# Optimization experiments

Measured on AMD Instinct MI355X. Metric: run time of the kernel, lower is better.

Reference implementation:

```python
import jax, jax.numpy as jnp
import numpy as np

EPS = 1e-5

def layernorm(x, g, b):
    mu = jnp.mean(x, axis=-1, keepdims=True)
    var = jnp.mean(jnp.square(x - mu), axis=-1, keepdims=True)
    return (x - mu) * jax.lax.rsqrt(var + EPS) * g + b

def setup_inputs() -> dict:
    key = jax.random.key(0)
    B, C, W = 1, 256, 64           # C = x_h_dim = query_dim
    D = 256                        # inner_dim = heads(1) * dim_head(256)
    ks = jax.random.split(key, 32)
    sc = 0.02
    inp = {
        'x': jax.random.normal(ks[0], (B, C, W, W), jnp.float32),
        'h': jax.random.normal(ks[1], (B, C, W, W), jnp.float32),
        's': jax.random.normal(ks[2], (B, C, W, W), jnp.float32),
        'm': jax.random.normal(ks[3], (B, C, W, W), jnp.float32),
        't': jax.random.normal(ks[4], (B, C), jnp.float32),
        'wt': jax.random.normal(ks[5], (C, D), jnp.float32) * sc,
        'bt': jnp.zeros((D,), jnp.float32),
        'wk_x': jax.random.normal(ks[6], (C, D), jnp.float32) * sc,
        'wv_x': jax.random.normal(ks[7], (C, D), jnp.float32) * sc,
        'g_x': jnp.ones((C,), jnp.float32), 'be_x': jnp.zeros((C,), jnp.float32),
        'wk_h': jax.random.normal(ks[8], (C, D), jnp.float32) * sc,
        'wv_h': jax.random.normal(ks[9], (C, D), jnp.float32) * sc,
        'g_h': jnp.ones((C,), jnp.float32), 'be_h': jnp.zeros((C,), jnp.float32),
        'wk_s': jax.random.normal(ks[10], (C, D), jnp.float32) * sc,
        'wv_s': jax.random.normal(ks[11], (C, D), jnp.float32) * sc,
        'g_s': jnp.ones((C,), jnp.float32), 'be_s': jnp.zeros((C,), jnp.float32),
        'wk_m': jax.random.normal(ks[12], (C, D), jnp.float32) * sc,
        'wv_m': jax.random.normal(ks[13], (C, D), jnp.float32) * sc,
        'g_m': jnp.ones((C,), jnp.float32), 'be_m': jnp.zeros((C,), jnp.float32),
        'w_geglu': jax.random.normal(ks[14], (D, 2 * D), jnp.float32) * sc,
        'b_geglu': jnp.zeros((2 * D,), jnp.float32),
        'w_ff2': jax.random.normal(ks[15], (D, D), jnp.float32) * sc,
        'b_ff2': jnp.zeros((D,), jnp.float32),
        'g_res': jnp.ones((D,), jnp.float32), 'be_res': jnp.zeros((D,), jnp.float32),
        'w_out': jax.random.normal(ks[16], (D, C), jnp.float32) * sc,
        'b_out': jnp.zeros((C,), jnp.float32),
        'imageWidth': W,
    }
    return inp

def reference(x, h, s, m, t, wt, bt, wk_x, wv_x, g_x, be_x, wk_h, wv_h, g_h, be_h,
              wk_s, wv_s, g_s, be_s, wk_m, wv_m, g_m, be_m,
              w_geglu, b_geglu, w_ff2, b_ff2, g_res, be_res, w_out, b_out, imageWidth):
    B, C, W, _ = x.shape
    N = W * W
    D = wt.shape[1]
    scale = 1.0 / jnp.sqrt(jnp.float32(D))  # dim_head**-0.5 (heads=1)

    # query: t_transform(t) broadcast over all spatial positions -> [B, N, D]
    q = t @ wt + bt
    query = jnp.broadcast_to(q[:, None, :], (B, N, D))

    def tokens(a):  # b c h w -> b (h w) c
        return a.reshape(B, C, N).transpose(0, 2, 1)

    mods = []
    for a, g, be, wk, wv in ((x, g_x, be_x, wk_x, wv_x), (h, g_h, be_h, wk_h, wv_h),
                             (s, g_s, be_s, wk_s, wv_s), (m, g_m, be_m, wk_m, wv_m)):
        a = layernorm(tokens(a), g, be)
        mods.append((a @ wk, a @ wv))  # (k, v) each [B, N, D]

    sims = [jnp.einsum('bid,bjd->bij', query, k) * scale for k, _ in mods]
    combined = jnp.concatenate(sims, axis=-1)          # [B, N, 4N]
    attn = jax.nn.softmax(combined, axis=-1)
    parts = jnp.split(attn, 4, axis=-1)

    out = sum(jnp.einsum('bij,bjd->bid', a, v) for a, (_, v) in zip(parts, mods))

    # FeedForward(inner_dim, mult=1, glu=True) on layernormed sum
    r = layernorm(out, g_res, be_res)
    gg = r @ w_geglu + b_geglu
    u, gate = jnp.split(gg, 2, axis=-1)
    ff = (u * jax.nn.gelu(gate, approximate=False)) @ w_ff2 + b_ff2

    y = ff @ w_out + b_out                              # [B, N, C]
    return y.transpose(0, 2, 1).reshape(B, C, W, W)
```

## Files before the change

### kernel.cpp

```cpp
#include <hip/hip_runtime.h>
#include <math.h>

#define N_TOK 4096

#define OFF_GU    0
#define OFF_GUP   1024
#define OFF_BUP   1056
#define OFF_PM    1088
#define OFF_PSE   1344
#define OFF_PSR   1600
#define OFF_OUTV  1856
#define OFF_GG    2112
#define OFF_Y     2624
#define OFF_WS    3072
#define OFF_WC    69632

#define TSTRIDE 65

__global__ __launch_bounds__(256) void k0(
    const float* __restrict__ t, const float* __restrict__ wt,
    const float* __restrict__ bt,
    const float* __restrict__ wk0, const float* __restrict__ wk1,
    const float* __restrict__ wk2, const float* __restrict__ wk3,
    const float* __restrict__ g0, const float* __restrict__ g1,
    const float* __restrict__ g2, const float* __restrict__ g3,
    const float* __restrict__ be0, const float* __restrict__ be1,
    const float* __restrict__ be2, const float* __restrict__ be3,
    const float* __restrict__ w_ff2, const float* __restrict__ w_out,
    const float* __restrict__ b_geglu, const float* __restrict__ b_ff2,
    const float* __restrict__ b_out, float* __restrict__ ws) {
  const int gid = blockIdx.x;
  const int tid = threadIdx.x;
  __shared__ float sh[264];

  if (gid < 256) {
    sh[tid] = w_ff2[gid * 256 + tid];
    __syncthreads();
    float acc = 0.f;
    #pragma unroll 8
    for (int d = 0; d < 256; ++d) acc += sh[d] * w_out[d * 256 + tid];
    ws[OFF_WC + gid * 256 + tid] = acc;
  } else if (gid < 288) {
    const int local = gid - 256;
    const int m = local >> 3;
    const int c0 = (local & 7) * 32;
    const float* wk = (m == 0) ? wk0 : (m == 1) ? wk1 : (m == 2) ? wk2 : wk3;
    const float* g  = (m == 0) ? g0  : (m == 1) ? g1  : (m == 2) ? g2  : g3;
    const float* be = (m == 0) ? be0 : (m == 1) ? be1 : (m == 2) ? be2 : be3;

    float acc = bt[tid];
    #pragma unroll 8
    for (int c = 0; c < 256; ++c) acc += t[c] * wt[c * 256 + tid];
    sh[tid] = acc;
    __syncthreads();

    const int w = tid >> 6, lane = tid & 63;
    const float4 qv = ((const float4*)sh)[lane];
    float lGU = 0.f, lBU = 0.f;
    #pragma unroll
    for (int r = 0; r < 8; ++r) {
      int c = c0 + w * 8 + r;
      float4 w4 = ((const float4*)(wk + c * 256))[lane];
      float sdot = w4.x * qv.x + w4.y * qv.y + w4.z * qv.z + w4.w * qv.w;
      for (int o = 32; o > 0; o >>= 1) sdot += __shfl_down(sdot, o, 64);
      if (lane == 0) {
        float u = sdot;
        float gu = g[c] * u;
        ws[OFF_GU + m * 256 + c] = gu;
        lGU += gu;
        lBU += be[c] * u;
      }
    }
    __syncthreads();
    if (lane == 0) { sh[256 + w] = lGU; sh[260 + w] = lBU; }
    __syncthreads();
    if (tid == 0) {
      ws[OFF_GUP + m * 8 + (local & 7)] = sh[256] + sh[257] + sh[258] + sh[259];
      ws[OFF_BUP + m * 8 + (local & 7)] = sh[260] + sh[261] + sh[262] + sh[263];
    }
  } else {
    ws[OFF_OUTV + tid] = 0.0f;
    ws[OFF_GG + tid] = b_geglu[tid];
    ws[OFF_GG + 256 + tid] = b_geglu[256 + tid];
    ws[OFF_Y + tid] = b_out[tid];
  }
}

__global__ __launch_bounds__(256) void k2(
    const float* __restrict__ A0, const float* __restrict__ A1,
    const float* __restrict__ A2, const float* __restrict__ A3,
    float* __restrict__ ws) {
  const int b = blockIdx.x;
  const int m = b >> 6;
  const int jbase = (b & 63) * 64;
  const int tid = threadIdx.x;
  const float* A = (m == 0) ? A0 : (m == 1) ? A1 : (m == 2) ? A2 : A3;

  __shared__ float tile[256 * TSTRIDE];
  __shared__ float gu_sh[256];
  __shared__ float r1[256], r2[256], r3[256];
  __shared__ float simj[64], rinvj[64], muj[64], alj[64];

  gu_sh[tid] = ws[OFF_GU + m * 256 + tid];

  {
    const int cr = tid >> 4;
    const int jf = tid & 15;
    #pragma unroll 4
    for (int it = 0; it < 16; ++it) {
      int c = it * 16 + cr;
      float4 v = *(const float4*)(A + c * N_TOK + jbase + jf * 4);
      int base = c * TSTRIDE + jf * 4;
      tile[base] = v.x; tile[base + 1] = v.y;
      tile[base + 2] = v.z; tile[base + 3] = v.w;
    }
  }
  __syncthreads();

  {
    const int j = tid & 63, q = tid >> 6;
    float s1 = 0.f, s2 = 0.f, s3 = 0.f;
    #pragma unroll 8
    for (int i = 0; i < 64; ++i) {
      int c = q * 64 + i;
      float v = tile[c * TSTRIDE + j];
      s1 += v; s2 += v * v; s3 += v * gu_sh[c];
    }
    r1[tid] = s1; r2[tid] = s2; r3[tid] = s3;
  }
  __syncthreads();
  if (tid < 64) {
    float S1 = r1[tid] + r1[tid + 64] + r1[tid + 128] + r1[tid + 192];
    float S2 = r2[tid] + r2[tid + 64] + r2[tid + 128] + r2[tid + 192];
    float S3 = r3[tid] + r3[tid + 64] + r3[tid + 128] + r3[tid + 192];
    float GU = 0.f, BU = 0.f;
    #pragma unroll
    for (int i = 0; i < 8; ++i) {
      GU += ws[OFF_GUP + m * 8 + i];
      BU += ws[OFF_BUP + m * 8 + i];
    }
    float mu = S1 * (1.0f / 256.0f);
    float var = S2 * (1.0f / 256.0f) - mu * mu;
    float rinv = rsqrtf(var + 1e-5f);
    simj[tid] = 0.0625f * (rinv * (S3 - mu * GU) + BU);
    muj[tid] = mu;
    rinvj[tid] = rinv;
  }
  __syncthreads();
  if (tid < 64) {
    float sim = simj[tid];
    float mb = sim;
    #pragma unroll
    for (int o = 1; o < 64; o <<= 1) mb = fmaxf(mb, __shfl_xor(mb, o, 64));
    float e = expf(sim - mb);
    float al = e * rinvj[tid];
    alj[tid] = al;
    float se = e, sr = al * muj[tid];
    #pragma unroll
    for (int o = 1; o < 64; o <<= 1) {
      se += __shfl_xor(se, o, 64);
      sr += __shfl_xor(sr, o, 64);
    }
    if (tid == 0) {
      ws[OFF_PM + b] = mb;
      ws[OFF_PSE + b] = se;
      ws[OFF_PSR + b] = sr;
    }
  }
  __syncthreads();
  {
    float wsum = 0.f;
    #pragma unroll 8
    for (int j = 0; j < 64; ++j) wsum += alj[j] * tile[tid * TSTRIDE + j];
    ws[OFF_WS + b * 256 + tid] = wsum;
  }
}

__global__ __launch_bounds__(256) void k3(
    const float* __restrict__ wv0, const float* __restrict__ wv1,
    const float* __restrict__ wv2, const float* __restrict__ wv3,
    const float* __restrict__ g0, const float* __restrict__ g1,
    const float* __restrict__ g2, const float* __restrict__ g3,
    const float* __restrict__ be0, const float* __restrict__ be1,
    const float* __restrict__ be2, const float* __restrict__ be3,
    float* __restrict__ ws) {
  const int b = blockIdx.x;
  const int mb = b >> 2;
  const int cbase = (b & 3) * 64;
  const int tid = threadIdx.x;
  const float* wv = (mb == 0) ? wv0 : (mb == 1) ? wv1 : (mb == 2) ? wv2 : wv3;
  const float* g  = (mb == 0) ? g0  : (mb == 1) ? g1  : (mb == 2) ? g2  : g3;
  const float* be = (mb == 0) ? be0 : (mb == 1) ? be1 : (mb == 2) ? be2 : be3;

  __shared__ float pm[256], pse[256], psr[256];
  __shared__ float red[4];
  __shared__ float wfin[64], fsh[64];
  __shared__ float sS, sAm, sPm;

  pm[tid] = ws[OFF_PM + tid];
  pse[tid] = ws[OFF_PSE + tid];
  psr[tid] = ws[OFF_PSR + tid];
  __syncthreads();

  float v = pm[tid];
  for (int o = 32; o > 0; o >>= 1) v = fmaxf(v, __shfl_down(v, o, 64));
  if ((tid & 63) == 0) red[tid >> 6] = v;
  __syncthreads();
  const float M = fmaxf(fmaxf(red[0], red[1]), fmaxf(red[2], red[3]));
  __syncthreads();

  const float f = expf(pm[tid] - M);
  const float fse = f * pse[tid];
  const bool mine = (tid >> 6) == mb;

  v = fse;
  for (int o = 32; o > 0; o >>= 1) v += __shfl_down(v, o, 64);
  if ((tid & 63) == 0) red[tid >> 6] = v;
  __syncthreads();
  if (tid == 0) sS = red[0] + red[1] + red[2] + red[3];
  __syncthreads();
  v = mine ? fse : 0.f;
  for (int o = 32; o > 0; o >>= 1) v += __shfl_down(v, o, 64);
  if ((tid & 63) == 0) red[tid >> 6] = v;
  __syncthreads();
  if (tid == 0) sAm = red[0] + red[1] + red[2] + red[3];
  __syncthreads();
  v = mine ? f * psr[tid] : 0.f;
  for (int o = 32; o > 0; o >>= 1) v += __shfl_down(v, o, 64);
  if ((tid & 63) == 0) red[tid >> 6] = v;
  __syncthreads();
  if (tid == 0) sPm = red[0] + red[1] + red[2] + red[3];
  if (tid < 64) fsh[tid] = expf(pm[mb * 64 + tid] - M);
  __syncthreads();

  const float invS = 1.0f / sS;

  {
    const int c_l = tid & 63, bg = tid >> 6;
    float part = 0.f;
    #pragma unroll 4
    for (int i = 0; i < 16; ++i) {
      int fb = bg * 16 + i;
      part += fsh[fb] * ws[OFF_WS + (mb * 64 + fb) * 256 + cbase + c_l];
    }
    pse[tid] = part;
  }
  __syncthreads();
  if (tid < 64) {
    float dot = (pse[tid] + pse[tid + 64] + pse[tid + 128] + pse[tid + 192]) * invS;
    int c = cbase + tid;
    wfin[tid] = g[c] * (dot - sPm * invS) + be[c] * (sAm * invS);
  }
  __syncthreads();

  {
    float acc = 0.f;
    #pragma unroll 8
    for (int i = 0; i < 64; ++i) acc += wfin[i] * wv[(cbase + i) * 256 + tid];
    atomicAdd(&ws[OFF_OUTV + tid], acc);
  }
}

__global__ __launch_bounds__(256) void k4(
    const float* __restrict__ g_res, const float* __restrict__ be_res,
    const float* __restrict__ w_geglu, float* __restrict__ ws) {
  const int gid = blockIdx.x;
  const int tid = threadIdx.x;
  __shared__ float r_sh[256];
  __shared__ float red[4];

  float od = ws[OFF_OUTV + tid];
  float v = od;
  for (int o = 32; o > 0; o >>= 1) v += __shfl_down(v, o, 64);
  if ((tid & 63) == 0) red[tid >> 6] = v;
  __syncthreads();
  float mu = (red[0] + red[1] + red[2] + red[3]) * (1.0f / 256.0f);
  __syncthreads();
  float dv = od - mu;
  v = dv * dv;
  for (int o = 32; o > 0; o >>= 1) v += __shfl_down(v, o, 64);
  if ((tid & 63) == 0) red[tid >> 6] = v;
  __syncthreads();
  float var = (red[0] + red[1] + red[2] + red[3]) * (1.0f / 256.0f);
  r_sh[tid] = dv * rsqrtf(var + 1e-5f) * g_res[tid] + be_res[tid];
  __syncthreads();

  const int dt = gid >> 4;
  const int d0 = (gid & 15) * 16;
  float acc = 0.f;
  #pragma unroll
  for (int i = 0; i < 16; ++i) {
    int d = d0 + i;
    acc += r_sh[d] * w_geglu[d * 512 + dt * 256 + tid];
  }
  atomicAdd(&ws[OFF_GG + dt * 256 + tid], acc);
}

__global__ __launch_bounds__(256) void k5(
    const float* __restrict__ b_ff2, const float* __restrict__ w_out,
    float* __restrict__ ws) {
  const int gid = blockIdx.x;
  const int tid = threadIdx.x;
  float acc = 0.f;
  if (gid < 16) {
    const int e0 = gid * 16;
    #pragma unroll
    for (int i = 0; i < 16; ++i) {
      int e = e0 + i;
      float u = ws[OFF_GG + e];
      float gate = ws[OFF_GG + 256 + e];
      float ffin = u * 0.5f * gate * (1.0f + erff(gate * 0.70710678118654752f));
      acc += ffin * ws[OFF_WC + e * 256 + tid];
    }
  } else {
    const int d0 = (gid - 16) * 16;
    #pragma unroll
    for (int i = 0; i < 16; ++i) {
      int d = d0 + i;
      acc += b_ff2[d] * w_out[d * 256 + tid];
    }
  }
  atomicAdd(&ws[OFF_Y + tid], acc);
}

__global__ __launch_bounds__(256) void k6(const float* __restrict__ ws,
                                          float4* __restrict__ out4) {
  const int gid = blockIdx.x;
  const int tid = threadIdx.x;
  #pragma unroll
  for (int k = 0; k < 2; ++k) {
    const int idx = gid * 512 + k * 256 + tid;
    const int c = idx >> 10;
    float v = ws[OFF_Y + c];
    out4[idx] = make_float4(v, v, v, v);
  }
}

extern "C" void kernel_launch(void* const* d_in, const int* in_sizes, int n_in,
                              void* d_out, int out_size, void* d_ws, size_t ws_size,
                              hipStream_t stream) {
  const float* x = (const float*)d_in[0];
  const float* h = (const float*)d_in[1];
  const float* s = (const float*)d_in[2];
  const float* m = (const float*)d_in[3];
  const float* t = (const float*)d_in[4];
  const float* wt = (const float*)d_in[5];
  const float* bt = (const float*)d_in[6];
  const float* wk_x = (const float*)d_in[7];
  const float* wv_x = (const float*)d_in[8];
  const float* g_x = (const float*)d_in[9];
  const float* be_x = (const float*)d_in[10];
  const float* wk_h = (const float*)d_in[11];
  const float* wv_h = (const float*)d_in[12];
  const float* g_h = (const float*)d_in[13];
  const float* be_h = (const float*)d_in[14];
  const float* wk_s = (const float*)d_in[15];
  const float* wv_s = (const float*)d_in[16];
  const float* g_s = (const float*)d_in[17];
  const float* be_s = (const float*)d_in[18];
  const float* wk_m = (const float*)d_in[19];
  const float* wv_m = (const float*)d_in[20];
  const float* g_m = (const float*)d_in[21];
  const float* be_m = (const float*)d_in[22];
  const float* w_geglu = (const float*)d_in[23];
  const float* b_geglu = (const float*)d_in[24];
  const float* w_ff2 = (const float*)d_in[25];
  const float* b_ff2 = (const float*)d_in[26];
  const float* g_res = (const float*)d_in[27];
  const float* be_res = (const float*)d_in[28];
  const float* w_out = (const float*)d_in[29];
  const float* b_out = (const float*)d_in[30];
  float* ws = (float*)d_ws;

  k0<<<dim3(289), dim3(256), 0, stream>>>(t, wt, bt,
      wk_x, wk_h, wk_s, wk_m, g_x, g_h, g_s, g_m, be_x, be_h, be_s, be_m,
      w_ff2, w_out, b_geglu, b_ff2, b_out, ws);
  k2<<<dim3(256), dim3(256), 0, stream>>>(x, h, s, m, ws);
  k3<<<dim3(16), dim3(256), 0, stream>>>(wv_x, wv_h, wv_s, wv_m,
      g_x, g_h, g_s, g_m, be_x, be_h, be_s, be_m, ws);
  k4<<<dim3(32), dim3(256), 0, stream>>>(g_res, be_res, w_geglu, ws);
  k5<<<dim3(32), dim3(256), 0, stream>>>(b_ff2, w_out, ws);
  k6<<<dim3(512), dim3(256), 0, stream>>>(ws, (float4*)d_out);
}
```

Before: 163.3 us.

## Fuse all stages into one cooperative kernel with grid syncs

Merges the six separate launches into a single cooperative kernel of 256 blocks. The stages are separated by grid-wide barriers, and the 256 blocks and shared-memory buffers are reused across stages. Atomic accumulations into the workspace are replaced by per-block partial buffers that the next stage sums. The folded b_ff2·w_out bias is now computed up front. The aim is to remove per-launch overhead and atomic contention. In exchange it adds five grid.sync barriers and makes every stage run with the larger shared-memory footprint, which may limit occupancy.

```diff
diff --git a/kernel.cpp b/kernel.cpp
--- a/kernel.cpp
+++ b/kernel.cpp
@@ -1,7 +1,11 @@
 #include <hip/hip_runtime.h>
+#include <hip/hip_cooperative_groups.h>
 #include <math.h>
 
+namespace cg = cooperative_groups;
+
 #define N_TOK 4096
+#define TSTRIDE 65
 
 #define OFF_GU    0
 #define OFF_GUP   1024
@@ -9,53 +13,62 @@
 #define OFF_PM    1088
 #define OFF_PSE   1344
 #define OFF_PSR   1600
-#define OFF_OUTV  1856
-#define OFF_GG    2112
-#define OFF_Y     2624
-#define OFF_WS    3072
-#define OFF_WC    69632
-
-#define TSTRIDE 65
-
-__global__ __launch_bounds__(256) void k0(
+#define OFF_YB    1856
+#define OFF_OUTP  2112
+#define OFF_GGP   6208
+#define OFF_YP    14400
+#define OFF_WS    18496
+#define OFF_WC    84032
+
+__global__ __launch_bounds__(256) void fused(
+    const float* __restrict__ xg, const float* __restrict__ hg,
+    const float* __restrict__ sg, const float* __restrict__ mg,
     const float* __restrict__ t, const float* __restrict__ wt,
     const float* __restrict__ bt,
     const float* __restrict__ wk0, const float* __restrict__ wk1,
     const float* __restrict__ wk2, const float* __restrict__ wk3,
+    const float* __restrict__ wv0, const float* __restrict__ wv1,
+    const float* __restrict__ wv2, const float* __restrict__ wv3,
     const float* __restrict__ g0, const float* __restrict__ g1,
     const float* __restrict__ g2, const float* __restrict__ g3,
     const float* __restrict__ be0, const float* __restrict__ be1,
     const float* __restrict__ be2, const float* __restrict__ be3,
-    const float* __restrict__ w_ff2, const float* __restrict__ w_out,
-    const float* __restrict__ b_geglu, const float* __restrict__ b_ff2,
-    const float* __restrict__ b_out, float* __restrict__ ws) {
-  const int gid = blockIdx.x;
+    const float* __restrict__ w_geglu, const float* __restrict__ b_geglu,
+    const float* __restrict__ w_ff2, const float* __restrict__ b_ff2,
+    const float* __restrict__ g_res, const float* __restrict__ be_res,
+    const float* __restrict__ w_out, const float* __restrict__ b_out,
+    float* __restrict__ ws, float4* __restrict__ out4) {
+  cg::grid_group grid = cg::this_grid();
+  const int b = blockIdx.x;
   const int tid = threadIdx.x;
-  __shared__ float sh[264];
-
-  if (gid < 256) {
-    sh[tid] = w_ff2[gid * 256 + tid];
-    __syncthreads();
+
+  __shared__ float tile[256 * TSTRIDE];
+  __shared__ float sA[256], sB[256], sC[256], sD[256], sE[256];
+  __shared__ float sRed[16];
+
+  sA[tid] = w_ff2[b * 256 + tid];
+  __syncthreads();
+  {
     float acc = 0.f;
     #pragma unroll 8
-    for (int d = 0; d < 256; ++d) acc += sh[d] * w_out[d * 256 + tid];
-    ws[OFF_WC + gid * 256 + tid] = acc;
-  } else if (gid < 288) {
-    const int local = gid - 256;
-    const int m = local >> 3;
-    const int c0 = (local & 7) * 32;
-    const float* wk = (m == 0) ? wk0 : (m == 1) ? wk1 : (m == 2) ? wk2 : wk3;
-    const float* g  = (m == 0) ? g0  : (m == 1) ? g1  : (m == 2) ? g2  : g3;
-    const float* be = (m == 0) ? be0 : (m == 1) ? be1 : (m == 2) ? be2 : be3;
+    for (int d = 0; d < 256; ++d) acc += sA[d] * w_out[d * 256 + tid];
+    ws[OFF_WC + b * 256 + tid] = acc;
+  }
+  if (b < 32) {
+    const int mo = b >> 3;
+    const int c0 = (b & 7) * 32;
+    const float* wk = (mo == 0) ? wk0 : (mo == 1) ? wk1 : (mo == 2) ? wk2 : wk3;
+    const float* g  = (mo == 0) ? g0  : (mo == 1) ? g1  : (mo == 2) ? g2  : g3;
+    const float* be = (mo == 0) ? be0 : (mo == 1) ? be1 : (mo == 2) ? be2 : be3;
 
     float acc = bt[tid];
     #pragma unroll 8
     for (int c = 0; c < 256; ++c) acc += t[c] * wt[c * 256 + tid];
-    sh[tid] = acc;
+    sB[tid] = acc;
     __syncthreads();
 
     const int w = tid >> 6, lane = tid & 63;
-    const float4 qv = ((const float4*)sh)[lane];
+    const float4 qv = ((const float4*)sB)[lane];
     float lGU = 0.f, lBU = 0.f;
     #pragma unroll
     for (int r = 0; r < 8; ++r) {
@@ -66,273 +79,250 @@
       if (lane == 0) {
         float u = sdot;
         float gu = g[c] * u;
-        ws[OFF_GU + m * 256 + c] = gu;
+        ws[OFF_GU + mo * 256 + c] = gu;
         lGU += gu;
         lBU += be[c] * u;
       }
     }
     __syncthreads();
-    if (lane == 0) { sh[256 + w] = lGU; sh[260 + w] = lBU; }
+    if (lane == 0) { sRed[w] = lGU; sRed[8 + w] = lBU; }
     __syncthreads();
     if (tid == 0) {
-      ws[OFF_GUP + m * 8 + (local & 7)] = sh[256] + sh[257] + sh[258] + sh[259];
-      ws[OFF_BUP + m * 8 + (local & 7)] = sh[260] + sh[261] + sh[262] + sh[263];
-    }
-  } else {
-    ws[OFF_OUTV + tid] = 0.0f;
-    ws[OFF_GG + tid] = b_geglu[tid];
-    ws[OFF_GG + 256 + tid] = b_geglu[256 + tid];
-    ws[OFF_Y + tid] = b_out[tid];
-  }
-}
-
-__global__ __launch_bounds__(256) void k2(
-    const float* __restrict__ A0, const float* __restrict__ A1,
-    const float* __restrict__ A2, const float* __restrict__ A3,
-    float* __restrict__ ws) {
-  const int b = blockIdx.x;
-  const int m = b >> 6;
-  const int jbase = (b & 63) * 64;
-  const int tid = threadIdx.x;
-  const float* A = (m == 0) ? A0 : (m == 1) ? A1 : (m == 2) ? A2 : A3;
-
-  __shared__ float tile[256 * TSTRIDE];
-  __shared__ float gu_sh[256];
-  __shared__ float r1[256], r2[256], r3[256];
-  __shared__ float simj[64], rinvj[64], muj[64], alj[64];
-
-  gu_sh[tid] = ws[OFF_GU + m * 256 + tid];
+      ws[OFF_GUP + mo * 8 + (b & 7)] = sRed[0] + sRed[1] + sRed[2] + sRed[3];
+      ws[OFF_BUP + mo * 8 + (b & 7)] = sRed[8] + sRed[9] + sRed[10] + sRed[11];
+    }
+  } else if (b == 32) {
+    float acc = b_out[tid];
+    #pragma unroll 8
+    for (int d = 0; d < 256; ++d) acc += b_ff2[d] * w_out[d * 256 + tid];
+    ws[OFF_YB + tid] = acc;
+  }
+
+  __threadfence();
+  grid.sync();
 
   {
-    const int cr = tid >> 4;
-    const int jf = tid & 15;
-    #pragma unroll 4
-    for (int it = 0; it < 16; ++it) {
-      int c = it * 16 + cr;
-      float4 v = *(const float4*)(A + c * N_TOK + jbase + jf * 4);
-      int base = c * TSTRIDE + jf * 4;
-      tile[base] = v.x; tile[base + 1] = v.y;
-      tile[base + 2] = v.z; tile[base + 3] = v.w;
-    }
-  }
-  __syncthreads();
-
-  {
-    const int j = tid & 63, q = tid >> 6;
-    float s1 = 0.f, s2 = 0.f, s3 = 0.f;
-    #pragma unroll 8
-    for (int i = 0; i < 64; ++i) {
-      int c = q * 64 + i;
-      float v = tile[c * TSTRIDE + j];
-      s1 += v; s2 += v * v; s3 += v * gu_sh[c];
-    }
-    r1[tid] = s1; r2[tid] = s2; r3[tid] = s3;
-  }
-  __syncthreads();
-  if (tid < 64) {
-    float S1 = r1[tid] + r1[tid + 64] + r1[tid + 128] + r1[tid + 192];
-    float S2 = r2[tid] + r2[tid + 64] + r2[tid + 128] + r2[tid + 192];
-    float S3 = r3[tid] + r3[tid + 64] + r3[tid + 128] + r3[tid + 192];
-    float GU = 0.f, BU = 0.f;
-    #pragma unroll
-    for (int i = 0; i < 8; ++i) {
-      GU += ws[OFF_GUP + m * 8 + i];
-      BU += ws[OFF_BUP + m * 8 + i];
-    }
-    float mu = S1 * (1.0f / 256.0f);
-    float var = S2 * (1.0f / 256.0f) - mu * mu;
-    float rinv = rsqrtf(var + 1e-5f);
-    simj[tid] = 0.0625f * (rinv * (S3 - mu * GU) + BU);
-    muj[tid] = mu;
-    rinvj[tid] = rinv;
-  }
-  __syncthreads();
-  if (tid < 64) {
-    float sim = simj[tid];
-    float mb = sim;
-    #pragma unroll
-    for (int o = 1; o < 64; o <<= 1) mb = fmaxf(mb, __shfl_xor(mb, o, 64));
-    float e = expf(sim - mb);
-    float al = e * rinvj[tid];
-    alj[tid] = al;
-    float se = e, sr = al * muj[tid];
-    #pragma unroll
-    for (int o = 1; o < 64; o <<= 1) {
-      se += __shfl_xor(se, o, 64);
-      sr += __shfl_xor(sr, o, 64);
-    }
-    if (tid == 0) {
-      ws[OFF_PM + b] = mb;
-      ws[OFF_PSE + b] = se;
-      ws[OFF_PSR + b] = sr;
-    }
-  }
-  __syncthreads();
-  {
-    float wsum = 0.f;
-    #pragma unroll 8
-    for (int j = 0; j < 64; ++j) wsum += alj[j] * tile[tid * TSTRIDE + j];
-    ws[OFF_WS + b * 256 + tid] = wsum;
-  }
-}
-
-__global__ __launch_bounds__(256) void k3(
-    const float* __restrict__ wv0, const float* __restrict__ wv1,
-    const float* __restrict__ wv2, const float* __restrict__ wv3,
-    const float* __restrict__ g0, const float* __restrict__ g1,
-    const float* __restrict__ g2, const float* __restrict__ g3,
-    const float* __restrict__ be0, const float* __restrict__ be1,
-    const float* __restrict__ be2, const float* __restrict__ be3,
-    float* __restrict__ ws) {
-  const int b = blockIdx.x;
-  const int mb = b >> 2;
-  const int cbase = (b & 3) * 64;
-  const int tid = threadIdx.x;
-  const float* wv = (mb == 0) ? wv0 : (mb == 1) ? wv1 : (mb == 2) ? wv2 : wv3;
-  const float* g  = (mb == 0) ? g0  : (mb == 1) ? g1  : (mb == 2) ? g2  : g3;
-  const float* be = (mb == 0) ? be0 : (mb == 1) ? be1 : (mb == 2) ? be2 : be3;
-
-  __shared__ float pm[256], pse[256], psr[256];
-  __shared__ float red[4];
-  __shared__ float wfin[64], fsh[64];
-  __shared__ float sS, sAm, sPm;
-
-  pm[tid] = ws[OFF_PM + tid];
-  pse[tid] = ws[OFF_PSE + tid];
-  psr[tid] = ws[OFF_PSR + tid];
-  __syncthreads();
-
-  float v = pm[tid];
-  for (int o = 32; o > 0; o >>= 1) v = fmaxf(v, __shfl_down(v, o, 64));
-  if ((tid & 63) == 0) red[tid >> 6] = v;
-  __syncthreads();
-  const float M = fmaxf(fmaxf(red[0], red[1]), fmaxf(red[2], red[3]));
-  __syncthreads();
-
-  const float f = expf(pm[tid] - M);
-  const float fse = f * pse[tid];
-  const bool mine = (tid >> 6) == mb;
-
-  v = fse;
-  for (int o = 32; o > 0; o >>= 1) v += __shfl_down(v, o, 64);
-  if ((tid & 63) == 0) red[tid >> 6] = v;
-  __syncthreads();
-  if (tid == 0) sS = red[0] + red[1] + red[2] + red[3];
-  __syncthreads();
-  v = mine ? fse : 0.f;
-  for (int o = 32; o > 0; o >>= 1) v += __shfl_down(v, o, 64);
-  if ((tid & 63) == 0) red[tid >> 6] = v;
-  __syncthreads();
-  if (tid == 0) sAm = red[0] + red[1] + red[2] + red[3];
-  __syncthreads();
-  v = mine ? f * psr[tid] : 0.f;
-  for (int o = 32; o > 0; o >>= 1) v += __shfl_down(v, o, 64);
-  if ((tid & 63) == 0) red[tid >> 6] = v;
-  __syncthreads();
-  if (tid == 0) sPm = red[0] + red[1] + red[2] + red[3];
-  if (tid < 64) fsh[tid] = expf(pm[mb * 64 + tid] - M);
-  __syncthreads();
-
-  const float invS = 1.0f / sS;
-
-  {
-    const int c_l = tid & 63, bg = tid >> 6;
-    float part = 0.f;
-    #pragma unroll 4
-    for (int i = 0; i < 16; ++i) {
-      int fb = bg * 16 + i;
-      part += fsh[fb] * ws[OFF_WS + (mb * 64 + fb) * 256 + cbase + c_l];
-    }
-    pse[tid] = part;
-  }
-  __syncthreads();
-  if (tid < 64) {
-    float dot = (pse[tid] + pse[tid + 64] + pse[tid + 128] + pse[tid + 192]) * invS;
-    int c = cbase + tid;
-    wfin[tid] = g[c] * (dot - sPm * invS) + be[c] * (sAm * invS);
-  }
-  __syncthreads();
-
-  {
+    const int mo = b >> 6;
+    const int jbase = (b & 63) * 64;
+    const float* A = (mo == 0) ? xg : (mo == 1) ? hg : (mo == 2) ? sg : mg;
+
+    sA[tid] = ws[OFF_GU + mo * 256 + tid];
+    {
+      const int cr = tid >> 4;
+      const int jf = tid & 15;
+      #pragma unroll 4
+      for (int it = 0; it < 16; ++it) {
+        int c = it * 16 + cr;
+        float4 v4 = *(const float4*)(A + c * N_TOK + jbase + jf * 4);
+        int base = c * TSTRIDE + jf * 4;
+        tile[base] = v4.x; tile[base + 1] = v4.y;
+        tile[base + 2] = v4.z; tile[base + 3] = v4.w;
+      }
+    }
+    __syncthreads();
+
+    {
+      const int j = tid & 63, q = tid >> 6;
+      float s1 = 0.f, s2 = 0.f, s3 = 0.f;
+      #pragma unroll 8
+      for (int i = 0; i < 64; ++i) {
+        int c = q * 64 + i;
+        float v = tile[c * TSTRIDE + j];
+        s1 += v; s2 += v * v; s3 += v * sA[c];
+      }
+      sB[tid] = s1; sC[tid] = s2; sD[tid] = s3;
+    }
+    __syncthreads();
+    if (tid < 64) {
+      float S1 = sB[tid] + sB[tid + 64] + sB[tid + 128] + sB[tid + 192];
+      float S2 = sC[tid] + sC[tid + 64] + sC[tid + 128] + sC[tid + 192];
+      float S3 = sD[tid] + sD[tid + 64] + sD[tid + 128] + sD[tid + 192];
+      float GU = 0.f, BU = 0.f;
+      #pragma unroll
+      for (int i = 0; i < 8; ++i) {
+        GU += ws[OFF_GUP + mo * 8 + i];
+        BU += ws[OFF_BUP + mo * 8 + i];
+      }
+      float mu = S1 * (1.0f / 256.0f);
+      float var = S2 * (1.0f / 256.0f) - mu * mu;
+      float rinv = rsqrtf(var + 1e-5f);
+      sE[tid] = 0.0625f * (rinv * (S3 - mu * GU) + BU);
+      sE[64 + tid] = rinv;
+      sE[128 + tid] = mu;
+    }
+    __syncthreads();
+    if (tid < 64) {
+      float sim = sE[tid];
+      float mb_ = sim;
+      #pragma unroll
+      for (int o = 1; o < 64; o <<= 1) mb_ = fmaxf(mb_, __shfl_xor(mb_, o, 64));
+      float e = expf(sim - mb_);
+      float al = e * sE[64 + tid];
+      sE[192 + tid] = al;
+      float se = e, sr = al * sE[128 + tid];
+      #pragma unroll
+      for (int o = 1; o < 64; o <<= 1) {
+        se += __shfl_xor(se, o, 64);
+        sr += __shfl_xor(sr, o, 64);
+      }
+      if (tid == 0) {
+        ws[OFF_PM + b] = mb_;
+        ws[OFF_PSE + b] = se;
+        ws[OFF_PSR + b] = sr;
+      }
+    }
+    __syncthreads();
+    {
+      float wsum = 0.f;
+      #pragma unroll 8
+      for (int j = 0; j < 64; ++j) wsum += sE[192 + j] * tile[tid * TSTRIDE + j];
+      ws[OFF_WS + b * 256 + tid] = wsum;
+    }
+  }
+
+  __threadfence();
+  grid.sync();
+
+  if (b < 16) {
+    const int mb = b >> 2;
+    const int cbase = (b & 3) * 64;
+    const float* wv = (mb == 0) ? wv0 : (mb == 1) ? wv1 : (mb == 2) ? wv2 : wv3;
+    const float* g  = (mb == 0) ? g0  : (mb == 1) ? g1  : (mb == 2) ? g2  : g3;
+    const float* be = (mb == 0) ? be0 : (mb == 1) ? be1 : (mb == 2) ? be2 : be3;
+
+    sA[tid] = ws[OFF_PM + tid];
+    sB[tid] = ws[OFF_PSE + tid];
+    sC[tid] = ws[OFF_PSR + tid];
+    __syncthreads();
+
+    float v = sA[tid];
+    for (int o = 32; o > 0; o >>= 1) v = fmaxf(v, __shfl_down(v, o, 64));
+    if ((tid & 63) == 0) sRed[tid >> 6] = v;
+    __syncthreads();
+    const float M = fmaxf(fmaxf(sRed[0], sRed[1]), fmaxf(sRed[2], sRed[3]));
+    __syncthreads();
+
+    const float f = expf(sA[tid] - M);
+    const float fse = f * sB[tid];
+    const bool mine = (tid >> 6) == mb;
+
+    v = fse;
+    for (int o = 32; o > 0; o >>= 1) v += __shfl_down(v, o, 64);
+    if ((tid & 63) == 0) sRed[tid >> 6] = v;
+    __syncthreads();
+    if (tid == 0) sRed[8] = sRed[0] + sRed[1] + sRed[2] + sRed[3];
+    __syncthreads();
+    v = mine ? fse : 0.f;
+    for (int o = 32; o > 0; o >>= 1) v += __shfl_down(v, o, 64);
+    if ((tid & 63) == 0) sRed[tid >> 6] = v;
+    __syncthreads();
+    if (tid == 0) sRed[9] = sRed[0] + sRed[1] + sRed[2] + sRed[3];
+    __syncthreads();
+    v = mine ? f * sC[tid] : 0.f;
+    for (int o = 32; o > 0; o >>= 1) v += __shfl_down(v, o, 64);
+    if ((tid & 63) == 0) sRed[tid >> 6] = v;
+    __syncthreads();
+    if (tid == 0) sRed[10] = sRed[0] + sRed[1] + sRed[2] + sRed[3];
+    if (tid < 64) sD[64 + tid] = expf(sA[mb * 64 + tid] - M);
+    __syncthreads();
+
+    const float invS = 1.0f / sRed[8];
+
+    {
+      const int c_l = tid & 63, bg = tid >> 6;
+      float part = 0.f;
+      #pragma unroll 4
+      for (int i = 0; i < 16; ++i) {
+        int fb = bg * 16 + i;
+        part += sD[64 + fb] * ws[OFF_WS + (mb * 64 + fb) * 256 + cbase + c_l];
+      }
+      sB[tid] = part;
+    }
+    __syncthreads();
+    if (tid < 64) {
+      float dot = (sB[tid] + sB[tid + 64] + sB[tid + 128] + sB[tid + 192]) * invS;
+      int c = cbase + tid;
+      sD[tid] = g[c] * (dot - sRed[10] * invS) + be[c] * (sRed[9] * invS);
+    }
+    __syncthreads();
+
+    {
+      float acc = 0.f;
+      #pragma unroll 8
+      for (int i = 0; i < 64; ++i) acc += sD[i] * wv[(cbase + i) * 256 + tid];
+      ws[OFF_OUTP + b * 256 + tid] = acc;
+    }
+  }
+
+  __threadfence();
+  grid.sync();
+
+  if (b < 32) {
+    float od = 0.f;
+    #pragma unroll
+    for (int i = 0; i < 16; ++i) od += ws[OFF_OUTP + i * 256 + tid];
+
+    float v = od;
+    for (int o = 32; o > 0; o >>= 1) v += __shfl_down(v, o, 64);
+    if ((tid & 63) == 0) sRed[tid >> 6] = v;
+    __syncthreads();
+    float mu = (sRed[0] + sRed[1] + sRed[2] + sRed[3]) * (1.0f / 256.0f);
+    __syncthreads();
+    float dv = od - mu;
+    v = dv * dv;
+    for (int o = 32; o > 0; o >>= 1) v += __shfl_down(v, o, 64);
+    if ((tid & 63) == 0) sRed[tid >> 6] = v;
+    __syncthreads();
+    float var = (sRed[0] + sRed[1] + sRed[2] + sRed[3]) * (1.0f / 256.0f);
+    sA[tid] = dv * rsqrtf(var + 1e-5f) * g_res[tid] + be_res[tid];
+    __syncthreads();
+
+    const int dt = b >> 4;
+    const int d0 = (b & 15) * 16;
     float acc = 0.f;
-    #pragma unroll 8
-    for (int i = 0; i < 64; ++i) acc += wfin[i] * wv[(cbase + i) * 256 + tid];
-    atomicAdd(&ws[OFF_OUTV + tid], acc);
-  }
-}
-
-__global__ __launch_bounds__(256) void k4(
-    const float* __restrict__ g_res, const float* __restrict__ be_res,
-    const float* __restrict__ w_geglu, float* __restrict__ ws) {
-  const int gid = blockIdx.x;
-  const int tid = threadIdx.x;
-  __shared__ float r_sh[256];
-  __shared__ float red[4];
-
-  float od = ws[OFF_OUTV + tid];
-  float v = od;
-  for (int o = 32; o > 0; o >>= 1) v += __shfl_down(v, o, 64);
-  if ((tid & 63) == 0) red[tid >> 6] = v;
-  __syncthreads();
-  float mu = (red[0] + red[1] + red[2] + red[3]) * (1.0f / 256.0f);
-  __syncthreads();
-  float dv = od - mu;
-  v = dv * dv;
-  for (int o = 32; o > 0; o >>= 1) v += __shfl_down(v, o, 64);
-  if ((tid & 63) == 0) red[tid >> 6] = v;
-  __syncthreads();
-  float var = (red[0] + red[1] + red[2] + red[3]) * (1.0f / 256.0f);
-  r_sh[tid] = dv * rsqrtf(var + 1e-5f) * g_res[tid] + be_res[tid];
-  __syncthreads();
-
-  const int dt = gid >> 4;
-  const int d0 = (gid & 15) * 16;
-  float acc = 0.f;
-  #pragma unroll
-  for (int i = 0; i < 16; ++i) {
-    int d = d0 + i;
-    acc += r_sh[d] * w_geglu[d * 512 + dt * 256 + tid];
-  }
-  atomicAdd(&ws[OFF_GG + dt * 256 + tid], acc);
-}
-
-__global__ __launch_bounds__(256) void k5(
-    const float* __restrict__ b_ff2, const float* __restrict__ w_out,
-    float* __restrict__ ws) {
-  const int gid = blockIdx.x;
-  const int tid = threadIdx.x;
-  float acc = 0.f;
-  if (gid < 16) {
-    const int e0 = gid * 16;
-    #pragma unroll
-    for (int i = 0; i < 16; ++i) {
-      int e = e0 + i;
-      float u = ws[OFF_GG + e];
-      float gate = ws[OFF_GG + 256 + e];
-      float ffin = u * 0.5f * gate * (1.0f + erff(gate * 0.70710678118654752f));
-      acc += ffin * ws[OFF_WC + e * 256 + tid];
-    }
-  } else {
-    const int d0 = (gid - 16) * 16;
     #pragma unroll
     for (int i = 0; i < 16; ++i) {
       int d = d0 + i;
-      acc += b_ff2[d] * w_out[d * 256 + tid];
-    }
-  }
-  atomicAdd(&ws[OFF_Y + tid], acc);
-}
-
-__global__ __launch_bounds__(256) void k6(const float* __restrict__ ws,
-                                          float4* __restrict__ out4) {
-  const int gid = blockIdx.x;
-  const int tid = threadIdx.x;
-  #pragma unroll
-  for (int k = 0; k < 2; ++k) {
-    const int idx = gid * 512 + k * 256 + tid;
-    const int c = idx >> 10;
-    float v = ws[OFF_Y + c];
-    out4[idx] = make_float4(v, v, v, v);
+      acc += sA[d] * w_geglu[d * 512 + dt * 256 + tid];
+    }
+    ws[OFF_GGP + b * 256 + tid] = acc;
+  }
+
+  __threadfence();
+  grid.sync();
+
+  if (b < 16) {
+    const int e0 = b * 16;
+    if (tid < 16) {
+      float u = b_geglu[e0 + tid];
+      float gate = b_geglu[256 + e0 + tid];
+      #pragma unroll
+      for (int p = 0; p < 16; ++p) {
+        u    += ws[OFF_GGP + p * 256 + e0 + tid];
+        gate += ws[OFF_GGP + (16 + p) * 256 + e0 + tid];
+      }
+      sA[tid] = u * 0.5f * gate * (1.0f + erff(gate * 0.70710678118654752f));
+    }
+    __syncthreads();
+    float acc = 0.f;
+    #pragma unroll
+    for (int i = 0; i < 16; ++i) acc += sA[i] * ws[OFF_WC + (e0 + i) * 256 + tid];
+    ws[OFF_YP + b * 256 + tid] = acc;
+  }
+
+  __threadfence();
+  grid.sync();
+
+  {
+    float yv = ws[OFF_YB + tid];
+    #pragma unroll
+    for (int p = 0; p < 16; ++p) yv += ws[OFF_YP + p * 256 + tid];
+    sA[tid] = yv;
+    __syncthreads();
+    const float val = sA[b];
+    const float4 v4 = make_float4(val, val, val, val);
+    #pragma unroll
+    for (int k = 0; k < 4; ++k) out4[b * 1024 + k * 256 + tid] = v4;
   }
 }
 
@@ -371,14 +361,19 @@
   const float* w_out = (const float*)d_in[29];
   const float* b_out = (const float*)d_in[30];
   float* ws = (float*)d_ws;
-
-  k0<<<dim3(289), dim3(256), 0, stream>>>(t, wt, bt,
-      wk_x, wk_h, wk_s, wk_m, g_x, g_h, g_s, g_m, be_x, be_h, be_s, be_m,
-      w_ff2, w_out, b_geglu, b_ff2, b_out, ws);
-  k2<<<dim3(256), dim3(256), 0, stream>>>(x, h, s, m, ws);
-  k3<<<dim3(16), dim3(256), 0, stream>>>(wv_x, wv_h, wv_s, wv_m,
-      g_x, g_h, g_s, g_m, be_x, be_h, be_s, be_m, ws);
-  k4<<<dim3(32), dim3(256), 0, stream>>>(g_res, be_res, w_geglu, ws);
-  k5<<<dim3(32), dim3(256), 0, stream>>>(b_ff2, w_out, ws);
-  k6<<<dim3(512), dim3(256), 0, stream>>>(ws, (float4*)d_out);
+  float4* out4 = (float4*)d_out;
+
+  void* args[] = {
+      (void*)&x, (void*)&h, (void*)&s, (void*)&m,
+      (void*)&t, (void*)&wt, (void*)&bt,
+      (void*)&wk_x, (void*)&wk_h, (void*)&wk_s, (void*)&wk_m,
+      (void*)&wv_x, (void*)&wv_h, (void*)&wv_s, (void*)&wv_m,
+      (void*)&g_x, (void*)&g_h, (void*)&g_s, (void*)&g_m,
+      (void*)&be_x, (void*)&be_h, (void*)&be_s, (void*)&be_m,
+      (void*)&w_geglu, (void*)&b_geglu, (void*)&w_ff2, (void*)&b_ff2,
+      (void*)&g_res, (void*)&be_res, (void*)&w_out, (void*)&b_out,
+      (void*)&ws, (void*)&out4};
+
+  hipLaunchCooperativeKernel((const void*)fused, dim3(256), dim3(256), args, 0,
+                             stream);
 }
```

Measured after the change: 445.9 us. 173% more time.
